# Performance work log

Hardware: AMD Instinct MI355X
Metric: run time of the kernel (lower is better)

## Reference

```python
import jax, jax.numpy as jnp
import numpy as np

B, T, D, E = 8, 2048, 256, 4
D_E = D // E


def setup_inputs() -> dict:
    key = jax.random.key(0)
    ks = jax.random.split(key, 12)
    s = 1.0 / np.sqrt(D)
    x = jax.random.normal(ks[0], (B, T, D), dtype=jnp.float32)
    # ensure max(seq_len) == T so the padded input matches this_batch_padlen
    seq_len = jnp.concatenate([
        jax.random.randint(ks[1], (B - 1,), T // 2, T),
        jnp.array([T]),
    ]).astype(jnp.int32)
    return {
        "x": x,
        "seq_len": seq_len,
        "wq": jax.random.uniform(ks[2], (D, D), jnp.float32, -s, s),
        "bq": jax.random.uniform(ks[3], (D,), jnp.float32, -s, s),
        "wk": jax.random.uniform(ks[4], (D, D), jnp.float32, -s, s),
        "bk": jax.random.uniform(ks[5], (D,), jnp.float32, -s, s),
        "wv": jax.random.uniform(ks[6], (D, D), jnp.float32, -s, s),
        "bv": jax.random.uniform(ks[7], (D,), jnp.float32, -s, s),
        "wo": jax.random.uniform(ks[8], (D, D), jnp.float32, -s, s),
        "bo": jax.random.uniform(ks[9], (D,), jnp.float32, -s, s),
        "theta": jnp.array([50.0], dtype=jnp.float32),
    }


def _split_heads(y):
    # faithful to torch: [B,T,D] -> permute(0,2,1) -> [B,D,T] -> reshape(B*E, T, D_E)
    return jnp.transpose(y, (0, 2, 1)).reshape(B * E, T, D_E)


def reference(x, seq_len, wq, bq, wk, bk, wv, bv, wo, bo, theta):
    Q = _split_heads(x @ wq.T + bq)          # [B*E, T, D_E]
    K = _split_heads(x @ wk.T + bk)          # [B*E, T, D_E]
    V = _split_heads(x @ wv.T + bv)          # [B*E, T, D_E]

    # padding mask: zero out query rows (and key cols) past seq_len[i]
    pos = jnp.arange(T)
    valid = (pos[None, :] < seq_len[:, None])                 # [B, T]
    mask_q = jnp.repeat(valid, E, axis=0).astype(Q.dtype)     # [B*E, T]
    Q = Q * mask_q[:, :, None]
    K = K * mask_q[:, :, None]

    scale = jnp.sqrt(jnp.float32(T))
    att = jnp.einsum('bqd,bkd->bqk', Q, K) / scale            # [B*E, T, T]

    # Gaussian positional penalty (is_punish=True)
    tpos = jnp.arange(T, dtype=jnp.float32)
    diff = tpos[None, :] - tpos[:, None]                      # j - i
    punish = jnp.exp(-(diff ** 2) / (theta[0] ** 2))          # [T, T]
    att = att * punish[None, :, :]

    att = jnp.where(att == 0.0, jnp.float32(-2e20), att)
    att = jax.nn.softmax(att, axis=2)

    ctx = jnp.einsum('bqk,bkd->bqd', att, V)                  # [B*E, T, D_E]
    # faithful inverse of _split_heads: permute(0,2,1)->reshape(B,D,T)->permute
    ctx = jnp.transpose(jnp.transpose(ctx, (0, 2, 1)).reshape(B, D, T), (0, 2, 1))
    A = ctx @ wo.T + bo
    return A + x
```

## Files before the change

kernel.cpp:

```cpp
#include <hip/hip_runtime.h>
#include <hip/hip_bf16.h>
#include <math.h>
#include <stdint.h>

#define B_SZ   8
#define T_SEQ  2048
#define DIM    256
#define NH     32
#define DE     64
#define BAND   509
#define M_ROWS (B_SZ * T_SEQ)

typedef __attribute__((ext_vector_type(8))) short short8;
typedef __attribute__((ext_vector_type(4))) float floatx4;
typedef __attribute__((ext_vector_type(4))) unsigned uintx4;
typedef unsigned short ushort_t;

__device__ __forceinline__ ushort_t f2bf(float x) {
    unsigned u = __float_as_uint(x);
    u += 0x7fffu + ((u >> 16) & 1u);
    return (ushort_t)(u >> 16);
}
__device__ __forceinline__ float bf2f(ushort_t b) {
    return __uint_as_float(((unsigned)b) << 16);
}
__device__ __forceinline__ unsigned pack2(float a, float b) {
    unsigned lo = __bfloat16_as_ushort(__float2bfloat16(a));
    unsigned hi = __bfloat16_as_ushort(__float2bfloat16(b));
    return lo | (hi << 16);
}

__device__ __forceinline__ double pd_exact(int d, float th) {
    float df  = (float)d;
    float arg = (-(df * df)) / (th * th);
    double pdd = exp((double)arg);
    if (pdd < 1.17549435082228751e-38)
        return rint(pdd * 0x1p149) * 0x1p-149;
    return (double)(float)pdd;
}

__global__ __launch_bounds__(256) void prep_kernel(
    const float* __restrict__ x,
    const float* __restrict__ wq, const float* __restrict__ wk,
    const float* __restrict__ wv, const float* __restrict__ wo,
    const float* __restrict__ theta,
    ushort_t* __restrict__ xb, ushort_t* __restrict__ wb,
    float* __restrict__ thr_g, float* __restrict__ pdf_g)
{
    const int bid = blockIdx.x, tid = threadIdx.x;
    if (bid < 2048) {
        size_t i8 = ((size_t)bid * 256 + tid) * 8;
        float4 a = *(const float4*)(x + i8);
        float4 b = *(const float4*)(x + i8 + 4);
        uint4 o;
        o.x = pack2(a.x, a.y); o.y = pack2(a.z, a.w);
        o.z = pack2(b.x, b.y); o.w = pack2(b.z, b.w);
        *(uint4*)(xb + i8) = o;
    } else if (bid < 2176) {
        size_t w8 = ((size_t)(bid - 2048) * 256 + tid) * 8;
        int which = (int)(w8 >> 16);
        const float* src = (which == 0) ? wq : (which == 1) ? wk : (which == 2) ? wv : wo;
        size_t off = w8 & 65535;
        float4 a = *(const float4*)(src + off);
        float4 b = *(const float4*)(src + off + 4);
        uint4 o;
        o.x = pack2(a.x, a.y); o.y = pack2(a.z, a.w);
        o.z = pack2(b.x, b.y); o.w = pack2(b.z, b.w);
        *(uint4*)(wb + w8) = o;
    } else {
        int i = (bid - 2176) * 256 + tid;
        float th = theta[0];
        if (i < 1024) {
            int d = i - 512;
            pdf_g[i] = (float)pd_exact(d, th) * 1.44269504088896340736f;
        }
        if (i < 1536) {
            int d = i - 768;
            int ad = d < 0 ? -d : d;
            if (ad < 321) {
                thr_g[i] = __builtin_inff();
            } else {
                double pdv = pd_exact(ad, th);
                thr_g[i] = (pdv == 0.0) ? __builtin_inff() : (float)(0x1p-150 / pdv);
            }
        }
    }
}

__global__ __launch_bounds__(256, 2) void proj_qkv_mfma(
    const ushort_t* __restrict__ xb, const ushort_t* __restrict__ wb,
    const float* __restrict__ bq, const float* __restrict__ bk,
    const float* __restrict__ bv, const int* __restrict__ seq_len,
    ushort_t* __restrict__ Qh, ushort_t* __restrict__ Kh, ushort_t* __restrict__ Vh)
{
    __shared__ __align__(16) ushort_t Ls[4][64][68];
    const int wave = threadIdx.x >> 6, lane = threadIdx.x & 63;
    const int quad = lane >> 4, l15 = lane & 15;
    const int task = blockIdx.x * 4 + wave;
    const int nt64 = task % 12;
    const int mstrip = task / 12;
    const int mode = nt64 >> 2;
    const int nloc_base = (nt64 & 3) * 64;
    const ushort_t* Wp = wb + (size_t)mode * 65536;
    const int m0 = mstrip * 64;
    const int bb = m0 >> 11;
    const int th0 = (m0 >> 6) & 31;
    const int sl = seq_len[bb];
    ushort_t* outp = (mode == 0) ? Qh : (mode == 1) ? Kh : Vh;
    const float* bias = (mode == 0) ? bq : (mode == 1) ? bk : bv;
    const int hh = bb * 4 + (nloc_base >> 6);
    const float oscale = (mode == 0) ? 0.022097086912079612f : 1.0f;

    short8 Bf[4][8];
    #pragma unroll
    for (int nt = 0; nt < 4; ++nt) {
        int nrow = nloc_base + nt * 16 + l15;
        #pragma unroll
        for (int ks = 0; ks < 8; ++ks)
            Bf[nt][ks] = *(const short8*)(Wp + (size_t)nrow * 256 + ks * 32 + quad * 8);
    }
    float bias4[4];
    #pragma unroll
    for (int nt = 0; nt < 4; ++nt) bias4[nt] = bias[nloc_base + nt * 16 + l15];

    short8 Acur[8];
    #pragma unroll
    for (int ks = 0; ks < 8; ++ks)
        Acur[ks] = *(const short8*)(xb + (size_t)(m0 + l15) * 256 + ks * 32 + quad * 8);

    #pragma unroll
    for (int mb = 0; mb < 4; ++mb) {
        const int mb0 = m0 + mb * 16;
        short8 Anext[8];
        if (mb < 3) {
            #pragma unroll
            for (int ks = 0; ks < 8; ++ks)
                Anext[ks] = *(const short8*)(xb + (size_t)(mb0 + 16 + l15) * 256 + ks * 32 + quad * 8);
        }
        floatx4 acc[4];
        #pragma unroll
        for (int nt = 0; nt < 4; ++nt) acc[nt] = (floatx4){0.f, 0.f, 0.f, 0.f};
        #pragma unroll
        for (int ks = 0; ks < 8; ++ks)
            #pragma unroll
            for (int nt = 0; nt < 4; ++nt)
                acc[nt] = __builtin_amdgcn_mfma_f32_16x16x32_bf16(Acur[ks], Bf[nt][ks], acc[nt], 0, 0, 0);
        #pragma unroll
        for (int nt = 0; nt < 4; ++nt) {
            float v0 = (acc[nt][0] + bias4[nt]) * oscale;
            float v1 = (acc[nt][1] + bias4[nt]) * oscale;
            float v2 = (acc[nt][2] + bias4[nt]) * oscale;
            float v3 = (acc[nt][3] + bias4[nt]) * oscale;
            uint2 pk; pk.x = pack2(v0, v1); pk.y = pack2(v2, v3);
            *(uint2*)&Ls[wave][nt * 16 + l15][mb * 16 + quad * 4] = pk;
        }
        #pragma unroll
        for (int ks = 0; ks < 8; ++ks) Acur[ks] = Anext[ks];
    }

    #pragma unroll
    for (int s = 0; s < 16; ++s) {
        int dl = s * 4 + quad;
        int e0 = l15 * 4;
        uint2 pk = *(const uint2*)&Ls[wave][dl][e0];
        int q = dl * 32 + th0;
        if (mode <= 1 && q >= sl) { pk.x = 0u; pk.y = 0u; }
        *(uint2*)(outp + (((size_t)hh * T_SEQ + q) << 6) + e0) = pk;
    }
}

__global__ __launch_bounds__(256) void vtrans_kernel(const ushort_t* __restrict__ Vh,
                                                     ushort_t* __restrict__ VTp,
                                                     float* __restrict__ mv)
{
    __shared__ ushort_t Vs[256][66];
    __shared__ float red[32][72];
    const int tid = threadIdx.x;
    const int h = blockIdx.x >> 3, chunk = blockIdx.x & 7;
    const ushort_t* src = Vh + ((size_t)(h * T_SEQ + chunk * 256)) * DE;
    float s[8] = {};
    #pragma unroll
    for (int rep = 0; rep < 8; ++rep) {
        int f = rep * 256 + tid;
        int row = f >> 3, c8 = (f & 7) * 8;
        uint4 u = *(const uint4*)(src + (size_t)row * DE + c8);
        *(uint4*)&Vs[row][c8] = u;
        const ushort_t* w = (const ushort_t*)&u;
        #pragma unroll
        for (int i = 0; i < 8; ++i) s[i] += bf2f(w[i]);
    }
    {
        const int r0 = tid >> 3, es = (tid & 7) * 8;
        #pragma unroll
        for (int i = 0; i < 8; ++i) red[r0][es + i] = s[i];
    }
    __syncthreads();
    if (tid < 64) {
        float t = 0.f;
        #pragma unroll
        for (int g = 0; g < 32; ++g) t += red[g][tid];
        atomicAdd(&mv[h * DE + tid], t);
    }
    const int w = tid >> 6, lane = tid & 63;
    const int half = lane >> 5;
    const int c32 = lane & 31;
    const int cbase = c32 * 8;
    const int blk = cbase >> 6;
    const int cin = cbase & 63;
    #pragma unroll
    for (int rr = 0; rr < 8; ++rr) {
        int e = w * 16 + rr * 2 + half;
        ushort_t tmp[8];
        #pragma unroll
        for (int t = 0; t < 8; ++t) {
            int ci = cin + t;
            int j = blk * 64 + 32 * (ci >> 5) + 4 * ((ci >> 3) & 3)
                  + 16 * ((ci >> 2) & 1) + (ci & 3);
            tmp[t] = Vs[j][e];
        }
        *(uint4*)(VTp + ((size_t)(h * DE + e)) * T_SEQ + chunk * 256 + cbase) = *(uint4*)tmp;
    }
}

__global__ __launch_bounds__(512) void attn_mfma_kernel(
    const ushort_t* __restrict__ Qh, const ushort_t* __restrict__ Kh,
    const ushort_t* __restrict__ VTp, const float* __restrict__ thr_g,
    const float* __restrict__ pdf_g, const float* __restrict__ mvs,
    const int* __restrict__ seq_len, ushort_t* __restrict__ ctxb)
{
    __shared__ ushort_t Ks [2][64][72];
    __shared__ ushort_t VTs[2][64][72];
    __shared__ float pdfl[1024];
    __shared__ float thrc[1536];

    const int tid  = threadIdx.x;
    const int wave = tid >> 6;
    const int lane = tid & 63;
    const int quad = lane >> 4;
    const int l15  = lane & 15;
    const int bid   = blockIdx.x;
    const int inner = bid >> 3;
    const int g     = inner >> 4;
    const int strip = ((inner & 15) + g * 4) & 15;
    const int h  = (g << 3) | (bid & 7);
    const int q0 = strip * 128;
    const int b  = h >> 2;
    const int sl = seq_len[b];
    const float invT = 1.0f / (float)T_SEQ;
    ushort_t* outbase = ctxb + ((size_t)b * T_SEQ + q0) * DIM + (size_t)(h & 3) * 64;

    if (q0 >= sl) {
        #pragma unroll
        for (int nt = 0; nt < 4; ++nt) {
            ushort_t mval = f2bf(mvs[h * DE + l15 + 16 * nt] * invT);
            #pragma unroll
            for (int r = 0; r < 4; ++r)
                outbase[(size_t)(wave * 16 + quad * 4 + r) * DIM + l15 + 16 * nt] = mval;
        }
        return;
    }

    for (int i = tid; i < 1024; i += 512) pdfl[i] = pdf_g[i];
    for (int i = tid; i < 1536; i += 512) thrc[i] = thr_g[i];

    short8 qa0, qa1;
    {
        const ushort_t* qp = Qh + ((size_t)h * T_SEQ + q0 + wave * 16 + l15) * DE + quad * 8;
        qa0 = *(const short8*)(qp);
        qa1 = *(const short8*)(qp + 32);
    }

    float l_acc = 0.f;
    floatx4 cacc[4];
    #pragma unroll
    for (int nt = 0; nt < 4; ++nt) cacc[nt] = (floatx4){0.f, 0.f, 0.f, 0.f};

    int jlo = q0 - BAND;       if (jlo < 0) jlo = 0;
    int jhi = q0 + 127 + BAND; if (jhi > sl - 1) jhi = sl - 1;
    const int jt0 = jlo >> 6, jt1 = jhi >> 6;

    const int krow = tid >> 3;
    const int kc8  = (tid & 7) * 8;
    const ushort_t* Kbp = Kh + (size_t)h * T_SEQ * DE;
    const ushort_t* Vbp = VTp + (size_t)h * DE * T_SEQ;
    uint4 kpre0, kpre1, vpre0, vpre1;
    {
        const int ja = jt0 << 6;
        const int jb = ((jt0 + 1 <= jt1) ? jt0 + 1 : jt1) << 6;
        kpre0 = *(const uint4*)(Kbp + (size_t)(ja + krow) * DE + kc8);
        vpre0 = *(const uint4*)(Vbp + (size_t)krow * T_SEQ + ja + kc8);
        kpre1 = *(const uint4*)(Kbp + (size_t)(jb + krow) * DE + kc8);
        vpre1 = *(const uint4*)(Vbp + (size_t)krow * T_SEQ + jb + kc8);
    }

    const int qrow = q0 + wave * 16 + l15;

    auto subtile = [&](int s, int j0s) {
        floatx4 ST[4];
        #pragma unroll
        for (int nt = 0; nt < 4; ++nt) {
            short8 ka0 = *(const short8*)&Ks[s][l15 + 16 * nt][quad * 8];
            short8 ka1 = *(const short8*)&Ks[s][l15 + 16 * nt][32 + quad * 8];
            floatx4 z = {0.f, 0.f, 0.f, 0.f};
            z = __builtin_amdgcn_mfma_f32_16x16x32_bf16(ka0, qa0, z, 0, 0, 0);
            z = __builtin_amdgcn_mfma_f32_16x16x32_bf16(ka1, qa1, z, 0, 0, 0);
            ST[nt] = z;
        }

        const int offw = j0s - q0 - wave * 16;
        const int db   = j0s + quad * 4 - qrow;
        float p[4][4];
        if (offw > -384 && offw < 336) {
            if (j0s + 63 < sl) {
                #pragma unroll
                for (int nt = 0; nt < 4; ++nt)
                    #pragma unroll
                    for (int r = 0; r < 4; ++r)
                        p[nt][r] = __builtin_amdgcn_exp2f(
                            ST[nt][r] * pdfl[db + 512 + nt * 16 + r]);
            } else {
                #pragma unroll
                for (int nt = 0; nt < 4; ++nt)
                    #pragma unroll
                    for (int r = 0; r < 4; ++r) {
                        float v = __builtin_amdgcn_exp2f(
                            ST[nt][r] * pdfl[db + 512 + nt * 16 + r]);
                        p[nt][r] = (j0s + nt * 16 + quad * 4 + r < sl) ? v : 0.f;
                    }
            }
        } else {
            #pragma unroll
            for (int nt = 0; nt < 4; ++nt)
                #pragma unroll
                for (int r = 0; r < 4; ++r)
                    p[nt][r] = (fabsf(ST[nt][r]) > thrc[db + 768 + nt * 16 + r])
                               ? 1.0f : 0.0f;
        }

        #pragma unroll
        for (int nt = 0; nt < 4; ++nt)
            l_acc += (p[nt][0] + p[nt][1]) + (p[nt][2] + p[nt][3]);

        uintx4 t0, t1;
        t0.x = pack2(p[0][0], p[0][1]); t0.y = pack2(p[0][2], p[0][3]);
        t0.z = pack2(p[1][0], p[1][1]); t0.w = pack2(p[1][2], p[1][3]);
        t1.x = pack2(p[2][0], p[2][1]); t1.y = pack2(p[2][2], p[2][3]);
        t1.z = pack2(p[3][0], p[3][1]); t1.w = pack2(p[3][2], p[3][3]);
        short8 pa0 = __builtin_bit_cast(short8, t0);
        short8 pa1 = __builtin_bit_cast(short8, t1);

        #pragma unroll
        for (int nt = 0; nt < 4; ++nt) {
            short8 vb0 = *(const short8*)&VTs[s][l15 + 16 * nt][quad * 8];
            short8 vb1 = *(const short8*)&VTs[s][l15 + 16 * nt][32 + quad * 8];
            floatx4 c = cacc[nt];
            c = __builtin_amdgcn_mfma_f32_16x16x32_bf16(pa0, vb0, c, 0, 0, 0);
            c = __builtin_amdgcn_mfma_f32_16x16x32_bf16(pa1, vb1, c, 0, 0, 0);
            cacc[nt] = c;
        }
    };

    for (int jt = jt0; jt <= jt1; jt += 2) {
        const int j0a = jt << 6;
        const bool has_b = (jt + 1 <= jt1);
        const int j0b = (has_b ? jt + 1 : jt1) << 6;
        __syncthreads();
        *(uint4*)&Ks [0][krow][kc8] = kpre0;
        *(uint4*)&VTs[0][krow][kc8] = vpre0;
        *(uint4*)&Ks [1][krow][kc8] = kpre1;
        *(uint4*)&VTs[1][krow][kc8] = vpre1;
        __syncthreads();
        if (jt + 2 <= jt1) {
            const int jn0 = (jt + 2) << 6;
            const int jn1 = ((jt + 3 <= jt1) ? jt + 3 : jt1) << 6;
            kpre0 = *(const uint4*)(Kbp + (size_t)(jn0 + krow) * DE + kc8);
            vpre0 = *(const uint4*)(Vbp + (size_t)krow * T_SEQ + jn0 + kc8);
            kpre1 = *(const uint4*)(Kbp + (size_t)(jn1 + krow) * DE + kc8);
            vpre1 = *(const uint4*)(Vbp + (size_t)krow * T_SEQ + jn1 + kc8);
        }
        subtile(0, j0a);
        if (has_b) subtile(1, j0b);
    }

    l_acc += __shfl_xor(l_acc, 16);
    l_acc += __shfl_xor(l_acc, 32);
    const float linv = 1.0f / l_acc;
    float linv4[4];
    #pragma unroll
    for (int r = 0; r < 4; ++r) linv4[r] = __shfl(linv, quad * 4 + r);

    #pragma unroll
    for (int nt = 0; nt < 4; ++nt) {
        #pragma unroll
        for (int r = 0; r < 4; ++r) {
            int row = wave * 16 + quad * 4 + r;
            int qg = q0 + row;
            float o = cacc[nt][r] * linv4[r];
            if (qg >= sl) o = mvs[h * DE + l15 + 16 * nt] * invT;
            outbase[(size_t)row * DIM + l15 + 16 * nt] = f2bf(o);
        }
    }
}

__global__ __launch_bounds__(256, 2) void proj_o_mfma(
    const ushort_t* __restrict__ ctx, const ushort_t* __restrict__ wb,
    const float* __restrict__ bo, const float* __restrict__ x,
    float* __restrict__ out)
{
    __shared__ __align__(16) ushort_t As[32][264];
    const int tid = threadIdx.x;
    const int wave = tid >> 6, lane = tid & 63;
    const int quad = lane >> 4, l15 = lane & 15;
    const int m0 = blockIdx.x * 32;
    const int n0 = wave * 64;
    const ushort_t* Wp = wb + (size_t)3 * 65536;

    #pragma unroll
    for (int rep = 0; rep < 4; ++rep) {
        int f = rep * 256 + tid;
        int row = f >> 5, c8 = (f & 31) * 8;
        *(uint4*)&As[row][c8] = *(const uint4*)(ctx + (size_t)(m0 + row) * 256 + c8);
    }

    short8 Bf[4][8];
    #pragma unroll
    for (int nt = 0; nt < 4; ++nt) {
        int nrow = n0 + nt * 16 + l15;
        #pragma unroll
        for (int ks = 0; ks < 8; ++ks)
            Bf[nt][ks] = *(const short8*)(Wp + (size_t)nrow * 256 + ks * 32 + quad * 8);
    }
    float bias4[4];
    #pragma unroll
    for (int nt = 0; nt < 4; ++nt) bias4[nt] = bo[n0 + nt * 16 + l15];

    __syncthreads();

    #pragma unroll
    for (int mb = 0; mb < 2; ++mb) {
        short8 Af[8];
        #pragma unroll
        for (int ks = 0; ks < 8; ++ks)
            Af[ks] = *(const short8*)&As[mb * 16 + l15][ks * 32 + quad * 8];
        floatx4 acc[4];
        #pragma unroll
        for (int nt = 0; nt < 4; ++nt) acc[nt] = (floatx4){0.f, 0.f, 0.f, 0.f};
        #pragma unroll
        for (int ks = 0; ks < 8; ++ks)
            #pragma unroll
            for (int nt = 0; nt < 4; ++nt)
                acc[nt] = __builtin_amdgcn_mfma_f32_16x16x32_bf16(Af[ks], Bf[nt][ks], acc[nt], 0, 0, 0);
        #pragma unroll
        for (int nt = 0; nt < 4; ++nt) {
            int d = n0 + nt * 16 + l15;
            #pragma unroll
            for (int r = 0; r < 4; ++r) {
                size_t mi = (size_t)(m0 + mb * 16 + quad * 4 + r) * 256 + d;
                out[mi] = acc[nt][r] + bias4[nt] + x[mi];
            }
        }
    }
}

extern "C" void kernel_launch(void* const* d_in, const int* in_sizes, int n_in,
                              void* d_out, int out_size, void* d_ws, size_t ws_size,
                              hipStream_t stream)
{
    (void)in_sizes; (void)n_in; (void)out_size; (void)ws_size;
    const float* x  = (const float*)d_in[0];
    const int*   sl = (const int*)d_in[1];
    const float* wq = (const float*)d_in[2];
    const float* bq = (const float*)d_in[3];
    const float* wk = (const float*)d_in[4];
    const float* bk = (const float*)d_in[5];
    const float* wv = (const float*)d_in[6];
    const float* bv = (const float*)d_in[7];
    const float* wo = (const float*)d_in[8];
    const float* bo = (const float*)d_in[9];
    const float* th = (const float*)d_in[10];
    float* out = (float*)d_out;

    char* ws = (char*)d_ws;
    const size_t SZH = (size_t)M_ROWS * DIM * sizeof(ushort_t);
    ushort_t* xb  = (ushort_t*)(ws);
    ushort_t* wb  = (ushort_t*)(ws + SZH);
    ushort_t* Qh  = (ushort_t*)(ws + SZH + 524288);
    ushort_t* Kh  = (ushort_t*)(ws + 2*SZH + 524288);
    ushort_t* Vh  = (ushort_t*)(ws + 3*SZH + 524288);
    ushort_t* VTp = (ushort_t*)(ws + 4*SZH + 524288);
    ushort_t* Cb  = (ushort_t*)(ws + 5*SZH + 524288);
    float*    Mv  = (float*)   (ws + 6*SZH + 524288);
    float*    Thr = (float*)   (ws + 6*SZH + 524288 + 8192);
    float*    Pdf = (float*)   (ws + 6*SZH + 524288 + 8192 + 6144);

    hipMemsetAsync(Mv, 0, NH * DE * sizeof(float), stream);
    prep_kernel<<<dim3(2186), dim3(256), 0, stream>>>(x, wq, wk, wv, wo, th, xb, wb, Thr, Pdf);
    proj_qkv_mfma<<<dim3(768), dim3(256), 0, stream>>>(xb, wb, bq, bk, bv, sl, Qh, Kh, Vh);
    vtrans_kernel<<<dim3(NH * 8), dim3(256), 0, stream>>>(Vh, VTp, Mv);
    attn_mfma_kernel<<<dim3(512), dim3(512), 0, stream>>>(Qh, Kh, VTp, Thr, Pdf, Mv, sl, Cb);
    proj_o_mfma<<<dim3(512), dim3(256), 0, stream>>>(Cb, wb, bo, x, out);
}
```

Measured before the change: 163.9 us.

## Process two query groups per wave in attention, halving block threads

The attention kernel now runs 4 waves of 256 threads instead of 8 waves of 512. Each wave handles 32 query rows as two 16-row groups, so every K and V fragment read from LDS feeds twice as many MFMAs. Each thread now loads two rows of each K/V tile, and accumulators and softmax sums are doubled. This cuts LDS read traffic and the number of waves sharing each barrier, at the cost of higher register pressure and less latency hiding per block.

```diff
diff --git a/kernel.cpp b/kernel.cpp
--- a/kernel.cpp
+++ b/kernel.cpp
@@ -222,7 +222,7 @@
     }
 }
 
-__global__ __launch_bounds__(512) void attn_mfma_kernel(
+__global__ __launch_bounds__(256) void attn_mfma_kernel(
     const ushort_t* __restrict__ Qh, const ushort_t* __restrict__ Kh,
     const ushort_t* __restrict__ VTp, const float* __restrict__ thr_g,
     const float* __restrict__ pdf_g, const float* __restrict__ mvs,
@@ -254,109 +254,129 @@
         for (int nt = 0; nt < 4; ++nt) {
             ushort_t mval = f2bf(mvs[h * DE + l15 + 16 * nt] * invT);
             #pragma unroll
-            for (int r = 0; r < 4; ++r)
-                outbase[(size_t)(wave * 16 + quad * 4 + r) * DIM + l15 + 16 * nt] = mval;
+            for (int qg = 0; qg < 2; ++qg)
+                #pragma unroll
+                for (int r = 0; r < 4; ++r)
+                    outbase[(size_t)(wave * 32 + qg * 16 + quad * 4 + r) * DIM + l15 + 16 * nt] = mval;
         }
         return;
     }
 
-    for (int i = tid; i < 1024; i += 512) pdfl[i] = pdf_g[i];
-    for (int i = tid; i < 1536; i += 512) thrc[i] = thr_g[i];
-
-    short8 qa0, qa1;
-    {
-        const ushort_t* qp = Qh + ((size_t)h * T_SEQ + q0 + wave * 16 + l15) * DE + quad * 8;
-        qa0 = *(const short8*)(qp);
-        qa1 = *(const short8*)(qp + 32);
-    }
-
-    float l_acc = 0.f;
-    floatx4 cacc[4];
-    #pragma unroll
-    for (int nt = 0; nt < 4; ++nt) cacc[nt] = (floatx4){0.f, 0.f, 0.f, 0.f};
+    for (int i = tid; i < 1024; i += 256) pdfl[i] = pdf_g[i];
+    for (int i = tid; i < 1536; i += 256) thrc[i] = thr_g[i];
+
+    short8 qa[2][2];
+    #pragma unroll
+    for (int qg = 0; qg < 2; ++qg) {
+        const ushort_t* qp = Qh + ((size_t)h * T_SEQ + q0 + wave * 32 + qg * 16 + l15) * DE + quad * 8;
+        qa[qg][0] = *(const short8*)(qp);
+        qa[qg][1] = *(const short8*)(qp + 32);
+    }
+
+    float l_acc[2] = {0.f, 0.f};
+    floatx4 cacc[2][4];
+    #pragma unroll
+    for (int qg = 0; qg < 2; ++qg)
+        #pragma unroll
+        for (int nt = 0; nt < 4; ++nt) cacc[qg][nt] = (floatx4){0.f, 0.f, 0.f, 0.f};
 
     int jlo = q0 - BAND;       if (jlo < 0) jlo = 0;
     int jhi = q0 + 127 + BAND; if (jhi > sl - 1) jhi = sl - 1;
     const int jt0 = jlo >> 6, jt1 = jhi >> 6;
 
-    const int krow = tid >> 3;
-    const int kc8  = (tid & 7) * 8;
+    const int kr  = tid >> 3;
+    const int kc8 = (tid & 7) * 8;
     const ushort_t* Kbp = Kh + (size_t)h * T_SEQ * DE;
     const ushort_t* Vbp = VTp + (size_t)h * DE * T_SEQ;
-    uint4 kpre0, kpre1, vpre0, vpre1;
+    uint4 pA_k0, pA_k1, pA_v0, pA_v1;
+    uint4 pB_k0, pB_k1, pB_v0, pB_v1;
     {
         const int ja = jt0 << 6;
         const int jb = ((jt0 + 1 <= jt1) ? jt0 + 1 : jt1) << 6;
-        kpre0 = *(const uint4*)(Kbp + (size_t)(ja + krow) * DE + kc8);
-        vpre0 = *(const uint4*)(Vbp + (size_t)krow * T_SEQ + ja + kc8);
-        kpre1 = *(const uint4*)(Kbp + (size_t)(jb + krow) * DE + kc8);
-        vpre1 = *(const uint4*)(Vbp + (size_t)krow * T_SEQ + jb + kc8);
-    }
-
-    const int qrow = q0 + wave * 16 + l15;
+        pA_k0 = *(const uint4*)(Kbp + (size_t)(ja + kr) * DE + kc8);
+        pA_k1 = *(const uint4*)(Kbp + (size_t)(ja + kr + 32) * DE + kc8);
+        pA_v0 = *(const uint4*)(Vbp + (size_t)kr * T_SEQ + ja + kc8);
+        pA_v1 = *(const uint4*)(Vbp + (size_t)(kr + 32) * T_SEQ + ja + kc8);
+        pB_k0 = *(const uint4*)(Kbp + (size_t)(jb + kr) * DE + kc8);
+        pB_k1 = *(const uint4*)(Kbp + (size_t)(jb + kr + 32) * DE + kc8);
+        pB_v0 = *(const uint4*)(Vbp + (size_t)kr * T_SEQ + jb + kc8);
+        pB_v1 = *(const uint4*)(Vbp + (size_t)(kr + 32) * T_SEQ + jb + kc8);
+    }
+
+    const int qrow0 = q0 + wave * 32 + l15;
 
     auto subtile = [&](int s, int j0s) {
-        floatx4 ST[4];
+        floatx4 ST[2][4];
         #pragma unroll
         for (int nt = 0; nt < 4; ++nt) {
             short8 ka0 = *(const short8*)&Ks[s][l15 + 16 * nt][quad * 8];
             short8 ka1 = *(const short8*)&Ks[s][l15 + 16 * nt][32 + quad * 8];
-            floatx4 z = {0.f, 0.f, 0.f, 0.f};
-            z = __builtin_amdgcn_mfma_f32_16x16x32_bf16(ka0, qa0, z, 0, 0, 0);
-            z = __builtin_amdgcn_mfma_f32_16x16x32_bf16(ka1, qa1, z, 0, 0, 0);
-            ST[nt] = z;
-        }
-
-        const int offw = j0s - q0 - wave * 16;
-        const int db   = j0s + quad * 4 - qrow;
-        float p[4][4];
-        if (offw > -384 && offw < 336) {
-            if (j0s + 63 < sl) {
+            #pragma unroll
+            for (int qg = 0; qg < 2; ++qg) {
+                floatx4 z = {0.f, 0.f, 0.f, 0.f};
+                z = __builtin_amdgcn_mfma_f32_16x16x32_bf16(ka0, qa[qg][0], z, 0, 0, 0);
+                z = __builtin_amdgcn_mfma_f32_16x16x32_bf16(ka1, qa[qg][1], z, 0, 0, 0);
+                ST[qg][nt] = z;
+            }
+        }
+
+        short8 pa[2][2];
+        #pragma unroll
+        for (int qg = 0; qg < 2; ++qg) {
+            const int offw = j0s - q0 - wave * 32 - qg * 16;
+            const int db   = j0s + quad * 4 - (qrow0 + qg * 16);
+            float p[4][4];
+            if (offw > -384 && offw < 336) {
+                if (j0s + 63 < sl) {
+                    #pragma unroll
+                    for (int nt = 0; nt < 4; ++nt)
+                        #pragma unroll
+                        for (int r = 0; r < 4; ++r)
+                            p[nt][r] = __builtin_amdgcn_exp2f(
+                                ST[qg][nt][r] * pdfl[db + 512 + nt * 16 + r]);
+                } else {
+                    #pragma unroll
+                    for (int nt = 0; nt < 4; ++nt)
+                        #pragma unroll
+                        for (int r = 0; r < 4; ++r) {
+                            float v = __builtin_amdgcn_exp2f(
+                                ST[qg][nt][r] * pdfl[db + 512 + nt * 16 + r]);
+                            p[nt][r] = (j0s + nt * 16 + quad * 4 + r < sl) ? v : 0.f;
+                        }
+                }
+            } else {
                 #pragma unroll
                 for (int nt = 0; nt < 4; ++nt)
                     #pragma unroll
                     for (int r = 0; r < 4; ++r)
-                        p[nt][r] = __builtin_amdgcn_exp2f(
-                            ST[nt][r] * pdfl[db + 512 + nt * 16 + r]);
-            } else {
-                #pragma unroll
-                for (int nt = 0; nt < 4; ++nt)
-                    #pragma unroll
-                    for (int r = 0; r < 4; ++r) {
-                        float v = __builtin_amdgcn_exp2f(
-                            ST[nt][r] * pdfl[db + 512 + nt * 16 + r]);
-                        p[nt][r] = (j0s + nt * 16 + quad * 4 + r < sl) ? v : 0.f;
-                    }
+                        p[nt][r] = (fabsf(ST[qg][nt][r]) > thrc[db + 768 + nt * 16 + r])
+                                   ? 1.0f : 0.0f;
             }
-        } else {
+
             #pragma unroll
             for (int nt = 0; nt < 4; ++nt)
-                #pragma unroll
-                for (int r = 0; r < 4; ++r)
-                    p[nt][r] = (fabsf(ST[nt][r]) > thrc[db + 768 + nt * 16 + r])
-                               ? 1.0f : 0.0f;
-        }
-
-        #pragma unroll
-        for (int nt = 0; nt < 4; ++nt)
-            l_acc += (p[nt][0] + p[nt][1]) + (p[nt][2] + p[nt][3]);
-
-        uintx4 t0, t1;
-        t0.x = pack2(p[0][0], p[0][1]); t0.y = pack2(p[0][2], p[0][3]);
-        t0.z = pack2(p[1][0], p[1][1]); t0.w = pack2(p[1][2], p[1][3]);
-        t1.x = pack2(p[2][0], p[2][1]); t1.y = pack2(p[2][2], p[2][3]);
-        t1.z = pack2(p[3][0], p[3][1]); t1.w = pack2(p[3][2], p[3][3]);
-        short8 pa0 = __builtin_bit_cast(short8, t0);
-        short8 pa1 = __builtin_bit_cast(short8, t1);
+                l_acc[qg] += (p[nt][0] + p[nt][1]) + (p[nt][2] + p[nt][3]);
+
+            uintx4 t0, t1;
+            t0.x = pack2(p[0][0], p[0][1]); t0.y = pack2(p[0][2], p[0][3]);
+            t0.z = pack2(p[1][0], p[1][1]); t0.w = pack2(p[1][2], p[1][3]);
+            t1.x = pack2(p[2][0], p[2][1]); t1.y = pack2(p[2][2], p[2][3]);
+            t1.z = pack2(p[3][0], p[3][1]); t1.w = pack2(p[3][2], p[3][3]);
+            pa[qg][0] = __builtin_bit_cast(short8, t0);
+            pa[qg][1] = __builtin_bit_cast(short8, t1);
+        }
 
         #pragma unroll
         for (int nt = 0; nt < 4; ++nt) {
             short8 vb0 = *(const short8*)&VTs[s][l15 + 16 * nt][quad * 8];
             short8 vb1 = *(const short8*)&VTs[s][l15 + 16 * nt][32 + quad * 8];
-            floatx4 c = cacc[nt];
-            c = __builtin_amdgcn_mfma_f32_16x16x32_bf16(pa0, vb0, c, 0, 0, 0);
-            c = __builtin_amdgcn_mfma_f32_16x16x32_bf16(pa1, vb1, c, 0, 0, 0);
-            cacc[nt] = c;
+            #pragma unroll
+            for (int qg = 0; qg < 2; ++qg) {
+                floatx4 c = cacc[qg][nt];
+                c = __builtin_amdgcn_mfma_f32_16x16x32_bf16(pa[qg][0], vb0, c, 0, 0, 0);
+                c = __builtin_amdgcn_mfma_f32_16x16x32_bf16(pa[qg][1], vb1, c, 0, 0, 0);
+                cacc[qg][nt] = c;
+            }
         }
     };
 
@@ -365,39 +385,51 @@
         const bool has_b = (jt + 1 <= jt1);
         const int j0b = (has_b ? jt + 1 : jt1) << 6;
         __syncthreads();
-        *(uint4*)&Ks [0][krow][kc8] = kpre0;
-        *(uint4*)&VTs[0][krow][kc8] = vpre0;
-        *(uint4*)&Ks [1][krow][kc8] = kpre1;
-        *(uint4*)&VTs[1][krow][kc8] = vpre1;
+        *(uint4*)&Ks [0][kr][kc8]      = pA_k0;
+        *(uint4*)&Ks [0][kr + 32][kc8] = pA_k1;
+        *(uint4*)&VTs[0][kr][kc8]      = pA_v0;
+        *(uint4*)&VTs[0][kr + 32][kc8] = pA_v1;
+        *(uint4*)&Ks [1][kr][kc8]      = pB_k0;
+        *(uint4*)&Ks [1][kr + 32][kc8] = pB_k1;
+        *(uint4*)&VTs[1][kr][kc8]      = pB_v0;
+        *(uint4*)&VTs[1][kr + 32][kc8] = pB_v1;
         __syncthreads();
         if (jt + 2 <= jt1) {
             const int jn0 = (jt + 2) << 6;
             const int jn1 = ((jt + 3 <= jt1) ? jt + 3 : jt1) << 6;
-            kpre0 = *(const uint4*)(Kbp + (size_t)(jn0 + krow) * DE + kc8);
-            vpre0 = *(const uint4*)(Vbp + (size_t)krow * T_SEQ + jn0 + kc8);
-            kpre1 = *(const uint4*)(Kbp + (size_t)(jn1 + krow) * DE + kc8);
-            vpre1 = *(const uint4*)(Vbp + (size_t)krow * T_SEQ + jn1 + kc8);
+            pA_k0 = *(const uint4*)(Kbp + (size_t)(jn0 + kr) * DE + kc8);
+            pA_k1 = *(const uint4*)(Kbp + (size_t)(jn0 + kr + 32) * DE + kc8);
+            pA_v0 = *(const uint4*)(Vbp + (size_t)kr * T_SEQ + jn0 + kc8);
+            pA_v1 = *(const uint4*)(Vbp + (size_t)(kr + 32) * T_SEQ + jn0 + kc8);
+            pB_k0 = *(const uint4*)(Kbp + (size_t)(jn1 + kr) * DE + kc8);
+            pB_k1 = *(const uint4*)(Kbp + (size_t)(jn1 + kr + 32) * DE + kc8);
+            pB_v0 = *(const uint4*)(Vbp + (size_t)kr * T_SEQ + jn1 + kc8);
+            pB_v1 = *(const uint4*)(Vbp + (size_t)(kr + 32) * T_SEQ + jn1 + kc8);
         }
         subtile(0, j0a);
         if (has_b) subtile(1, j0b);
     }
 
-    l_acc += __shfl_xor(l_acc, 16);
-    l_acc += __shfl_xor(l_acc, 32);
-    const float linv = 1.0f / l_acc;
-    float linv4[4];
-    #pragma unroll
-    for (int r = 0; r < 4; ++r) linv4[r] = __shfl(linv, quad * 4 + r);
-
-    #pragma unroll
-    for (int nt = 0; nt < 4; ++nt) {
-        #pragma unroll
-        for (int r = 0; r < 4; ++r) {
-            int row = wave * 16 + quad * 4 + r;
-            int qg = q0 + row;
-            float o = cacc[nt][r] * linv4[r];
-            if (qg >= sl) o = mvs[h * DE + l15 + 16 * nt] * invT;
-            outbase[(size_t)row * DIM + l15 + 16 * nt] = f2bf(o);
+    #pragma unroll
+    for (int qg = 0; qg < 2; ++qg) {
+        float lv = l_acc[qg];
+        lv += __shfl_xor(lv, 16);
+        lv += __shfl_xor(lv, 32);
+        const float linv = 1.0f / lv;
+        float linv4[4];
+        #pragma unroll
+        for (int r = 0; r < 4; ++r) linv4[r] = __shfl(linv, quad * 4 + r);
+
+        #pragma unroll
+        for (int nt = 0; nt < 4; ++nt) {
+            #pragma unroll
+            for (int r = 0; r < 4; ++r) {
+                int row = wave * 32 + qg * 16 + quad * 4 + r;
+                int qgl = q0 + row;
+                float o = cacc[qg][nt][r] * linv4[r];
+                if (qgl >= sl) o = mvs[h * DE + l15 + 16 * nt] * invT;
+                outbase[(size_t)row * DIM + l15 + 16 * nt] = f2bf(o);
+            }
         }
     }
 }
@@ -497,6 +529,6 @@
     prep_kernel<<<dim3(2186), dim3(256), 0, stream>>>(x, wq, wk, wv, wo, th, xb, wb, Thr, Pdf);
     proj_qkv_mfma<<<dim3(768), dim3(256), 0, stream>>>(xb, wb, bq, bk, bv, sl, Qh, Kh, Vh);
     vtrans_kernel<<<dim3(NH * 8), dim3(256), 0, stream>>>(Vh, VTp, Mv);
-    attn_mfma_kernel<<<dim3(512), dim3(512), 0, stream>>>(Qh, Kh, VTp, Thr, Pdf, Mv, sl, Cb);
+    attn_mfma_kernel<<<dim3(512), dim3(256), 0, stream>>>(Qh, Kh, VTp, Thr, Pdf, Mv, sl, Cb);
     proj_o_mfma<<<dim3(512), dim3(256), 0, stream>>>(Cb, wb, bo, x, out);
 }
```

New measurement: 169.3 us. 3.3% more time.
